# Kernel tuning notes

Hardware: AMD Instinct MI355X
Metric: run time of the kernel (lower is better)

The kernel has to match this reference:

```python
import jax, jax.numpy as jnp
import numpy as np

B, N, D = 32, 128, 64
E = N * N
EPS = 1e-5


def _bn(x, gamma, beta):
    # torch BatchNorm1d on (B, C, D): normalize per-channel over (batch, last dim)
    mean = jnp.mean(x, axis=(0, 2), keepdims=True)
    var = jnp.var(x, axis=(0, 2), keepdims=True)
    return (x - mean) * jax.lax.rsqrt(var + EPS) * gamma[None, :, None] + beta[None, :, None]


def _gat_layer(x, edge, Wh, We, Wp, Wa, gv, bv, ge, be):
    b, n, d = x.shape
    res = x
    z_h = jnp.einsum('bnd,od->bno', x, Wh)   # fc_h (torch Linear: y = x W^T)
    z_e = jnp.einsum('bed,od->beo', edge, We)  # fc_e
    # incidence matmuls are pure gathers: edge e = i*n + j
    z_src = jnp.broadcast_to(z_h[:, None, :, :], (b, n, n, d)).reshape(b, n * n, d)  # start: edge (i,j) <- node j
    z_dst = jnp.broadcast_to(z_h[:, :, None, :], (b, n, n, d)).reshape(b, n * n, d)  # end:   edge (i,j) <- node i
    z = jnp.concatenate([z_src, z_dst, z_e], axis=-1)  # (b, E, 3d)
    z_e_new = jnp.einsum('bec,oc->beo', z, Wp)  # fc_proj
    attn = jnp.einsum('bec,c->be', z, Wa[0])    # attn_fc -> (b, E)
    attn = jnp.where(attn >= 0, attn, 0.01 * attn)  # LeakyReLU(0.01)
    attn = jax.nn.softmax(attn.reshape(b, n, n), axis=2).reshape(b, n * n)  # softmax over sources j
    # scatter via end^T: node i <- sum_j attn[i,j] * z_src[i*n+j]
    agg = (attn[:, :, None] * z_src).reshape(b, n, n, d).sum(axis=2)
    x_new = jax.nn.elu(res + _bn(agg, gv, bv))
    edge_new = jax.nn.elu(_bn(z_e_new, ge, be))
    return x_new, edge_new


def setup_inputs():
    key = jax.random.key(0)
    ks = jax.random.split(key, 10)
    scale = float(np.sqrt(2.0 / D))
    return {
        'x': jax.random.normal(ks[0], (B, N, D), jnp.float32),
        'edge': jax.random.normal(ks[1], (B, E, D), jnp.float32),
        'Wh1': jax.random.normal(ks[2], (D, D), jnp.float32) * scale,
        'We1': jax.random.normal(ks[3], (D, D), jnp.float32) * scale,
        'Wp1': jax.random.normal(ks[4], (D, 3 * D), jnp.float32) * scale,
        'Wa1': jax.random.normal(ks[5], (1, 3 * D), jnp.float32) * scale,
        'Wh2': jax.random.normal(ks[6], (D, D), jnp.float32) * scale,
        'We2': jax.random.normal(ks[7], (D, D), jnp.float32) * scale,
        'Wp2': jax.random.normal(ks[8], (D, 3 * D), jnp.float32) * scale,
        'Wa2': jax.random.normal(ks[9], (1, 3 * D), jnp.float32) * scale,
        'gv1': jnp.ones((N,), jnp.float32), 'bv1': jnp.zeros((N,), jnp.float32),
        'ge1': jnp.ones((E,), jnp.float32), 'be1': jnp.zeros((E,), jnp.float32),
        'gv2': jnp.ones((N,), jnp.float32), 'bv2': jnp.zeros((N,), jnp.float32),
        'ge2': jnp.ones((E,), jnp.float32), 'be2': jnp.zeros((E,), jnp.float32),
    }


def reference(x, edge, Wh1, We1, Wp1, Wa1, Wh2, We2, Wp2, Wa2,
              gv1, bv1, ge1, be1, gv2, bv2, ge2, be2):
    x, edge = _gat_layer(x, edge, Wh1, We1, Wp1, Wa1, gv1, bv1, ge1, be1)
    x, edge = _gat_layer(x, edge, Wh2, We2, Wp2, Wa2, gv2, bv2, ge2, be2)
    return x, edge
```

## Files before the change

### kernel.cpp

```cpp
#include <hip/hip_runtime.h>
#include <math.h>

#define BB 32
#define NN 128
#define DD 64
#define EE (NN*NN)
#define EPSI 1e-5f

typedef __attribute__((ext_vector_type(8))) short bf16x8;
typedef __attribute__((ext_vector_type(4))) short s16x4;
typedef __attribute__((ext_vector_type(4))) float f32x4;

#define LGKM0() do { asm volatile("s_waitcnt lgkmcnt(0)" ::: "memory"); \
                     __builtin_amdgcn_sched_barrier(0); } while (0)

__device__ __forceinline__ short f2bf(float f) {
    union { float f; unsigned u; } v; v.f = f;
    unsigned u = v.u;
    unsigned r = (u + 0x7FFFu + ((u >> 16) & 1u)) >> 16;
    return (short)r;
}
__device__ __forceinline__ float elu(float v) {
    return v > 0.f ? v : __expf(v) - 1.f;
}

__global__ void k_node(const float* __restrict__ x, const float* __restrict__ Wh,
                       const float* __restrict__ Wp, const float* __restrict__ We,
                       const float* __restrict__ Wa,
                       float* __restrict__ zh, float* __restrict__ PsT,
                       float* __restrict__ PdT, float* __restrict__ sO,
                       float* __restrict__ tO,
                       short* __restrict__ MbT, short* __restrict__ wfT)
{
    const int row = blockIdx.x;
    const int d = threadIdx.x;
    if (row >= BB*NN) {
        const int ff = row - BB*NN;
        float acc = 0.f;
        for (int o = 0; o < DD; ++o)
            acc += Wp[ff*192 + 128 + o] * We[o*DD + d];
        MbT[(((ff >> 4)*2 + (d >> 5))*64 + (ff & 15) + ((d >> 3) & 3)*16)*8 + (d & 7)]
            = f2bf(acc);
        if (ff == 0) {
            for (int q = 0; q < 16; ++q) wfT[d*16 + q] = 0;
            __syncthreads();
            float aw = 0.f;
            for (int o = 0; o < DD; ++o)
                aw += Wa[128 + o] * We[o*DD + d];
            wfT[((d >> 5)*64 + ((d >> 3) & 3)*16)*8 + (d & 7)] = f2bf(aw);
        }
        return;
    }
    const int b = row >> 7, n = row & 127;
    __shared__ float xr[DD];
    __shared__ float zr[DD];
    xr[d] = x[row*DD + d];
    __syncthreads();
    float acc = 0.f;
#pragma unroll
    for (int k = 0; k < DD; ++k) acc += xr[k] * Wh[d*DD + k];
    zr[d] = acc;
    zh[row*DD + d] = acc;
    __syncthreads();
    float a0 = 0.f, a1 = 0.f;
#pragma unroll
    for (int o = 0; o < DD; ++o) {
        float z = zr[o];
        a0 += Wp[d*192 + o]      * z;
        a1 += Wp[d*192 + 64 + o] * z;
    }
    const int fi = ((b >> 4)*4 + (d >> 4))*256 + (((b >> 2) & 3)*16 + (d & 15))*4 + (b & 3);
    PsT[n*2048 + fi] = a0;
    PdT[n*2048 + fi] = a1;
    float sv = zr[d] * Wa[d];
    float tv = zr[d] * Wa[64 + d];
#pragma unroll
    for (int off = 32; off; off >>= 1) {
        sv += __shfl_xor(sv, off);
        tv += __shfl_xor(tv, off);
    }
    if (d == 0) { sO[row] = sv; tO[row] = tv; }
}

template <int INM, int OUTM>
__global__ __launch_bounds__(256, 4) void k_edge(
    const void* einv,
    const short* __restrict__ MbT,
    const short* __restrict__ wfT,
    const float* __restrict__ PsT,
    const float* __restrict__ PdT,
    const float* __restrict__ ge, const float* __restrict__ be,
    void* eoutv, float* __restrict__ uout)
{
    __shared__ short As[4][32][72];
    const int t  = threadIdx.x;
    const int l  = t & 63;
    const int wv = t >> 6;
    const int lr = l & 15;
    const int lg = l >> 4;
    const int e0 = blockIdx.x * 4;
    const int e  = e0 + wv;
    const int i0 = e >> 7, j0 = e & 127;

    bf16x8 afr[2][2];
    if constexpr (INM == 0) {
        const float* ein = (const float*)einv;
        const int tq = (t >> 4) & 3;
        const int d0 = (t & 15) * 4;
        float4 sv[8];
#pragma unroll
        for (int it = 0; it < 8; ++it) {
            const int b = it*4 + wv;
            sv[it] = *reinterpret_cast<const float4*>(
                         ein + ((size_t)b*EE + e0 + tq)*DD + d0);
        }
#pragma unroll
        for (int it = 0; it < 8; ++it) {
            const int b = it*4 + wv;
            s16x4 o;
            o[0] = f2bf(sv[it].x); o[1] = f2bf(sv[it].y);
            o[2] = f2bf(sv[it].z); o[3] = f2bf(sv[it].w);
            *reinterpret_cast<s16x4*>(&As[tq][b][d0]) = o;
        }
        __syncthreads();
#pragma unroll
        for (int m = 0; m < 2; ++m)
#pragma unroll
            for (int s = 0; s < 2; ++s)
                afr[m][s] = *reinterpret_cast<const bf16x8*>(
                                &As[wv][16*m + lr][s*32 + lg*8]);
    } else {
        const short* ein = (const short*)einv + (size_t)e*BB*DD;
#pragma unroll
        for (int m = 0; m < 2; ++m)
#pragma unroll
            for (int s = 0; s < 2; ++s)
                afr[m][s] = *reinterpret_cast<const bf16x8*>(
                                ein + ((m*2 + s)*64 + l)*8);
    }

    bf16x8 bfr[4][2];
#pragma unroll
    for (int n = 0; n < 4; ++n)
#pragma unroll
        for (int s = 0; s < 2; ++s)
            bfr[n][s] = *reinterpret_cast<const bf16x8*>(MbT + ((n*2 + s)*64 + l)*8);
    bf16x8 wfrag[2];
#pragma unroll
    for (int s = 0; s < 2; ++s)
        wfrag[s] = *reinterpret_cast<const bf16x8*>(wfT + (s*64 + l)*8);

    f32x4 acc[2][4];
    f32x4 uacc[2];
    {
        const float* psb = PsT + j0*2048;
        const float* pdb = PdT + i0*2048;
#pragma unroll
        for (int m = 0; m < 2; ++m) {
            uacc[m] = (f32x4){0.f, 0.f, 0.f, 0.f};
#pragma unroll
            for (int n = 0; n < 4; ++n) {
                const float4 a = *reinterpret_cast<const float4*>(psb + (m*4+n)*256 + l*4);
                const float4 c = *reinterpret_cast<const float4*>(pdb + (m*4+n)*256 + l*4);
                acc[m][n] = (f32x4){a.x+c.x, a.y+c.y, a.z+c.z, a.w+c.w};
            }
        }
    }

#pragma unroll
    for (int m = 0; m < 2; ++m) {
#pragma unroll
        for (int n = 0; n < 4; ++n)
            acc[m][n] = __builtin_amdgcn_mfma_f32_16x16x32_bf16(afr[m][0], bfr[n][0], acc[m][n], 0, 0, 0);
        uacc[m] = __builtin_amdgcn_mfma_f32_16x16x32_bf16(afr[m][0], wfrag[0], uacc[m], 0, 0, 0);
#pragma unroll
        for (int n = 0; n < 4; ++n)
            acc[m][n] = __builtin_amdgcn_mfma_f32_16x16x32_bf16(afr[m][1], bfr[n][1], acc[m][n], 0, 0, 0);
        uacc[m] = __builtin_amdgcn_mfma_f32_16x16x32_bf16(afr[m][1], wfrag[1], uacc[m], 0, 0, 0);
    }

    float s1 = 0.f, s2 = 0.f;
#pragma unroll
    for (int m = 0; m < 2; ++m)
#pragma unroll
        for (int n = 0; n < 4; ++n)
#pragma unroll
            for (int q = 0; q < 4; ++q) { float v = acc[m][n][q]; s1 += v; s2 += v*v; }
#pragma unroll
    for (int off = 1; off < 64; off <<= 1) {
        s1 += __shfl_xor(s1, off);
        s2 += __shfl_xor(s2, off);
    }
    const float mean = s1 * (1.f/2048.f);
    const float var  = s2 * (1.f/2048.f) - mean*mean;
    const float sc = ge[e] * rsqrtf(var + EPSI);
    const float sh = be[e] - mean*sc;

#pragma unroll
    for (int m = 0; m < 2; ++m)
#pragma unroll
        for (int n = 0; n < 4; ++n)
#pragma unroll
            for (int q = 0; q < 4; ++q)
                acc[m][n][q] = elu(acc[m][n][q]*sc + sh);

    if (lr == 0) {
#pragma unroll
        for (int m = 0; m < 2; ++m)
#pragma unroll
            for (int q = 0; q < 4; ++q)
                uout[(size_t)(16*m + 4*lg + q)*EE + e] = uacc[m][q];
    }

    float (*Z)[68] = reinterpret_cast<float (*)[68]>(&As[wv][0][0]);
    LGKM0();
#pragma unroll
    for (int h = 0; h < 2; ++h) {
#pragma unroll
        for (int n = 0; n < 4; ++n)
#pragma unroll
            for (int q = 0; q < 4; ++q)
                Z[4*lg + q][16*n + lr] = acc[h][n][q];
        LGKM0();
        if constexpr (OUTM == 0) {
            float* eout = (float*)eoutv;
#pragma unroll
            for (int it = 0; it < 4; ++it) {
                const int rr = lg + 4*it;
                const int b  = 16*h + rr;
                float4 z = *reinterpret_cast<float4*>(&Z[rr][lr*4]);
                *reinterpret_cast<float4*>(eout + ((size_t)b*EE + e)*DD + lr*4) = z;
            }
        } else {
            short* eoutp = (short*)eoutv + (size_t)e*BB*DD;
#pragma unroll
            for (int it = 0; it < 2; ++it) {
                const int rr = (l >> 3) + 8*it;
                const int c0 = (l & 7)*8;
                float4 zlo = *reinterpret_cast<float4*>(&Z[rr][c0]);
                float4 zhi = *reinterpret_cast<float4*>(&Z[rr][c0+4]);
                bf16x8 o;
                o[0]=f2bf(zlo.x); o[1]=f2bf(zlo.y); o[2]=f2bf(zlo.z); o[3]=f2bf(zlo.w);
                o[4]=f2bf(zhi.x); o[5]=f2bf(zhi.y); o[6]=f2bf(zhi.z); o[7]=f2bf(zhi.w);
                const int sp = (l & 7) >> 2;
                const int lp = rr + ((l & 3) << 4);
                *reinterpret_cast<bf16x8*>(eoutp + ((h*2 + sp)*64 + lp)*8) = o;
            }
        }
        LGKM0();
    }
}

__global__ void k_attn(const float* __restrict__ sI, const float* __restrict__ tI,
                       const float* __restrict__ u, const float* __restrict__ zh,
                       float* __restrict__ agg)
{
    int blk = blockIdx.x; int b = blk >> 7, i = blk & 127;
    int l = threadIdx.x;
    __shared__ float at[NN];
    float ti = tI[blk];
    float l0 = sI[b*NN + l]      + ti + u[b*EE + i*NN + l];
    float l1 = sI[b*NN + l + 64] + ti + u[b*EE + i*NN + l + 64];
    l0 = l0 >= 0.f ? l0 : 0.01f*l0;
    l1 = l1 >= 0.f ? l1 : 0.01f*l1;
    float mx = fmaxf(l0, l1);
#pragma unroll
    for (int off = 32; off; off >>= 1) mx = fmaxf(mx, __shfl_xor(mx, off));
    float e0 = __expf(l0 - mx), e1 = __expf(l1 - mx);
    float sm = e0 + e1;
#pragma unroll
    for (int off = 32; off; off >>= 1) sm += __shfl_xor(sm, off);
    float inv = 1.f / sm;
    at[l]      = e0 * inv;
    at[l + 64] = e1 * inv;
    __syncthreads();
    const float* zb = zh + (size_t)b*NN*DD + l;
    float a0 = 0.f, a1 = 0.f, a2 = 0.f, a3 = 0.f;
#pragma unroll 4
    for (int j = 0; j < NN; j += 4) {
        a0 += at[j]     * zb[(j)    *DD];
        a1 += at[j + 1] * zb[(j + 1)*DD];
        a2 += at[j + 2] * zb[(j + 2)*DD];
        a3 += at[j + 3] * zb[(j + 3)*DD];
    }
    agg[(b*NN + i)*DD + l] = (a0 + a1) + (a2 + a3);
}

__global__ void k_vbn(const float* __restrict__ agg, const float* __restrict__ xres,
                      const float* __restrict__ gv, const float* __restrict__ bv,
                      float* __restrict__ xout)
{
    int i = blockIdx.x, t = threadIdx.x;
    float vals[8];
    float s1 = 0.f, s2 = 0.f;
#pragma unroll
    for (int q = 0; q < 8; ++q) {
        int m = t + 256*q; int b = m >> 6, d = m & 63;
        float v = agg[(b*NN + i)*DD + d];
        vals[q] = v; s1 += v; s2 += v*v;
    }
#pragma unroll
    for (int off = 1; off < 64; off <<= 1) {
        s1 += __shfl_xor(s1, off);
        s2 += __shfl_xor(s2, off);
    }
    __shared__ float r1[4], r2[4];
    int wv = t >> 6;
    if ((t & 63) == 0) { r1[wv] = s1; r2[wv] = s2; }
    __syncthreads();
    s1 = r1[0] + r1[1] + r1[2] + r1[3];
    s2 = r2[0] + r2[1] + r2[2] + r2[3];
    float mean  = s1 * (1.f/2048.f);
    float var   = s2 * (1.f/2048.f) - mean*mean;
    float scale = gv[i] * rsqrtf(var + EPSI);
    float shift = bv[i] - mean*scale;
#pragma unroll
    for (int q = 0; q < 8; ++q) {
        int m = t + 256*q; int b = m >> 6, d = m & 63;
        float v = vals[q]*scale + shift + xres[(b*NN + i)*DD + d];
        xout[(b*NN + i)*DD + d] = v > 0.f ? v : __expf(v) - 1.f;
    }
}

extern "C" void kernel_launch(void* const* d_in, const int* in_sizes, int n_in,
                              void* d_out, int out_size, void* d_ws, size_t ws_size,
                              hipStream_t stream)
{
    const float* x    = (const float*)d_in[0];
    const float* edge = (const float*)d_in[1];
    const float* Wh1  = (const float*)d_in[2];
    const float* We1  = (const float*)d_in[3];
    const float* Wp1  = (const float*)d_in[4];
    const float* Wa1  = (const float*)d_in[5];
    const float* Wh2  = (const float*)d_in[6];
    const float* We2  = (const float*)d_in[7];
    const float* Wp2  = (const float*)d_in[8];
    const float* Wa2  = (const float*)d_in[9];
    const float* gv1  = (const float*)d_in[10];
    const float* bv1  = (const float*)d_in[11];
    const float* ge1  = (const float*)d_in[12];
    const float* be1  = (const float*)d_in[13];
    const float* gv2  = (const float*)d_in[14];
    const float* bv2  = (const float*)d_in[15];
    const float* ge2  = (const float*)d_in[16];
    const float* be2  = (const float*)d_in[17];

    float* xout = (float*)d_out;
    float* eout = (float*)d_out + BB*NN*DD;

    float* ws  = (float*)d_ws;
    short* MbT = (short*)ws;  ws += DD*DD/2;
    short* wfT = (short*)ws;  ws += 1024/2;
    float* zh  = ws;  ws += BB*NN*DD;
    float* PsT = ws;  ws += NN*BB*DD;
    float* PdT = ws;  ws += NN*BB*DD;
    float* sb  = ws;  ws += BB*NN;
    float* tb  = ws;  ws += BB*NN;
    float* ub  = ws;  ws += BB*EE;
    float* agg = ws;  ws += BB*NN*DD;
    float* x1  = ws;  ws += BB*NN*DD;
    short* ebf = (short*)ws;
    const size_t need = ((size_t)(ws - (float*)d_ws))*4 + (size_t)EE*BB*DD*2;

    const bool dense = (ws_size >= need);

    k_node<<<BB*NN + 64, 64, 0, stream>>>(x, Wh1, Wp1, We1, Wa1, zh, PsT, PdT, sb, tb, MbT, wfT);
    if (dense)
        k_edge<0,1><<<EE/4, 256, 0, stream>>>(edge, MbT, wfT, PsT, PdT, ge1, be1, ebf, ub);
    else
        k_edge<0,0><<<EE/4, 256, 0, stream>>>(edge, MbT, wfT, PsT, PdT, ge1, be1, eout, ub);
    k_attn<<<BB*NN, 64, 0, stream>>>(sb, tb, ub, zh, agg);
    k_vbn<<<NN, 256, 0, stream>>>(agg, x, gv1, bv1, x1);
    k_node<<<BB*NN + 64, 64, 0, stream>>>(x1, Wh2, Wp2, We2, Wa2, zh, PsT, PdT, sb, tb, MbT, wfT);
    if (dense)
        k_edge<1,0><<<EE/4, 256, 0, stream>>>(ebf, MbT, wfT, PsT, PdT, ge2, be2, eout, ub);
    else
        k_edge<0,0><<<EE/4, 256, 0, stream>>>(eout, MbT, wfT, PsT, PdT, ge2, be2, eout, ub);
    k_attn<<<BB*NN, 64, 0, stream>>>(sb, tb, ub, zh, agg);
    k_vbn<<<NN, 256, 0, stream>>>(agg, x1, gv2, bv2, xout);
}
```

Before: 182.7 us.

## Make k_edge waves independent, use DPP reductions and single-pass output staging

Each wave now loads its own edge's 32x64 input tile instead of the block cooperatively loading four edges. This removes the block-wide __syncthreads, and the per-wave shared region is enlarged so all 32 rows of the fp32 output fit at once, which makes the epilogue one pass. The 64-lane shuffle-xor reductions for the batch-norm statistics are replaced with DPP row shifts/broadcasts plus readlane. The trade-off is a different global load pattern: each wave reads 16 lanes per contiguous 256-byte row instead of the previous coalescing across 4 adjacent edges, plus a larger LDS footprint per block.

Result: slower. 187.6 us (+2.7%).

```diff
diff --git a/kernel.cpp b/kernel.cpp
--- a/kernel.cpp
+++ b/kernel.cpp
@@ -13,6 +13,20 @@
 
 #define LGKM0() do { asm volatile("s_waitcnt lgkmcnt(0)" ::: "memory"); \
                      __builtin_amdgcn_sched_barrier(0); } while (0)
+
+#define DPPADD(v, ctrl, rmask)                                               \
+    (v) += __int_as_float(__builtin_amdgcn_update_dpp(                       \
+               0, __float_as_int(v), (ctrl), (rmask), 0xf, true))
+
+__device__ __forceinline__ float wave_sum64(float v) {
+    DPPADD(v, 0x111, 0xf);
+    DPPADD(v, 0x112, 0xf);
+    DPPADD(v, 0x114, 0xf);
+    DPPADD(v, 0x118, 0xf);
+    DPPADD(v, 0x142, 0xa);
+    DPPADD(v, 0x143, 0xc);
+    return __int_as_float(__builtin_amdgcn_readlane(__float_as_int(v), 63));
+}
 
 __device__ __forceinline__ short f2bf(float f) {
     union { float f; unsigned u; } v; v.f = f;
@@ -92,43 +106,42 @@
     const float* __restrict__ ge, const float* __restrict__ be,
     void* eoutv, float* __restrict__ uout)
 {
-    __shared__ short As[4][32][72];
+    __shared__ __align__(16) char SM[4][8704];
     const int t  = threadIdx.x;
     const int l  = t & 63;
     const int wv = t >> 6;
     const int lr = l & 15;
     const int lg = l >> 4;
-    const int e0 = blockIdx.x * 4;
-    const int e  = e0 + wv;
+    const int e  = blockIdx.x * 4 + wv;
     const int i0 = e >> 7, j0 = e & 127;
+    short (*As)[72] = reinterpret_cast<short (*)[72]>(&SM[wv][0]);
+    float (*Z)[68]  = reinterpret_cast<float (*)[68]>(&SM[wv][0]);
 
     bf16x8 afr[2][2];
     if constexpr (INM == 0) {
         const float* ein = (const float*)einv;
-        const int tq = (t >> 4) & 3;
-        const int d0 = (t & 15) * 4;
         float4 sv[8];
 #pragma unroll
         for (int it = 0; it < 8; ++it) {
-            const int b = it*4 + wv;
+            const int b = 4*it + (l >> 4);
             sv[it] = *reinterpret_cast<const float4*>(
-                         ein + ((size_t)b*EE + e0 + tq)*DD + d0);
+                         ein + ((size_t)b*EE + e)*DD + (l & 15)*4);
         }
 #pragma unroll
         for (int it = 0; it < 8; ++it) {
-            const int b = it*4 + wv;
+            const int b = 4*it + (l >> 4);
             s16x4 o;
             o[0] = f2bf(sv[it].x); o[1] = f2bf(sv[it].y);
             o[2] = f2bf(sv[it].z); o[3] = f2bf(sv[it].w);
-            *reinterpret_cast<s16x4*>(&As[tq][b][d0]) = o;
-        }
-        __syncthreads();
+            *reinterpret_cast<s16x4*>(&As[b][(l & 15)*4]) = o;
+        }
+        LGKM0();
 #pragma unroll
         for (int m = 0; m < 2; ++m)
 #pragma unroll
             for (int s = 0; s < 2; ++s)
                 afr[m][s] = *reinterpret_cast<const bf16x8*>(
-                                &As[wv][16*m + lr][s*32 + lg*8]);
+                                &As[16*m + lr][s*32 + lg*8]);
     } else {
         const short* ein = (const short*)einv + (size_t)e*BB*DD;
 #pragma unroll
@@ -186,11 +199,8 @@
         for (int n = 0; n < 4; ++n)
 #pragma unroll
             for (int q = 0; q < 4; ++q) { float v = acc[m][n][q]; s1 += v; s2 += v*v; }
-#pragma unroll
-    for (int off = 1; off < 64; off <<= 1) {
-        s1 += __shfl_xor(s1, off);
-        s2 += __shfl_xor(s2, off);
-    }
+    s1 = wave_sum64(s1);
+    s2 = wave_sum64(s2);
     const float mean = s1 * (1.f/2048.f);
     const float var  = s2 * (1.f/2048.f) - mean*mean;
     const float sc = ge[e] * rsqrtf(var + EPSI);
@@ -212,42 +222,38 @@
                 uout[(size_t)(16*m + 4*lg + q)*EE + e] = uacc[m][q];
     }
 
-    float (*Z)[68] = reinterpret_cast<float (*)[68]>(&As[wv][0][0]);
     LGKM0();
 #pragma unroll
-    for (int h = 0; h < 2; ++h) {
+    for (int m = 0; m < 2; ++m)
 #pragma unroll
         for (int n = 0; n < 4; ++n)
 #pragma unroll
             for (int q = 0; q < 4; ++q)
-                Z[4*lg + q][16*n + lr] = acc[h][n][q];
-        LGKM0();
-        if constexpr (OUTM == 0) {
-            float* eout = (float*)eoutv;
-#pragma unroll
-            for (int it = 0; it < 4; ++it) {
-                const int rr = lg + 4*it;
-                const int b  = 16*h + rr;
-                float4 z = *reinterpret_cast<float4*>(&Z[rr][lr*4]);
-                *reinterpret_cast<float4*>(eout + ((size_t)b*EE + e)*DD + lr*4) = z;
-            }
-        } else {
-            short* eoutp = (short*)eoutv + (size_t)e*BB*DD;
-#pragma unroll
-            for (int it = 0; it < 2; ++it) {
-                const int rr = (l >> 3) + 8*it;
-                const int c0 = (l & 7)*8;
-                float4 zlo = *reinterpret_cast<float4*>(&Z[rr][c0]);
-                float4 zhi = *reinterpret_cast<float4*>(&Z[rr][c0+4]);
-                bf16x8 o;
-                o[0]=f2bf(zlo.x); o[1]=f2bf(zlo.y); o[2]=f2bf(zlo.z); o[3]=f2bf(zlo.w);
-                o[4]=f2bf(zhi.x); o[5]=f2bf(zhi.y); o[6]=f2bf(zhi.z); o[7]=f2bf(zhi.w);
-                const int sp = (l & 7) >> 2;
-                const int lp = rr + ((l & 3) << 4);
-                *reinterpret_cast<bf16x8*>(eoutp + ((h*2 + sp)*64 + lp)*8) = o;
-            }
-        }
-        LGKM0();
+                Z[16*m + 4*lg + q][16*n + lr] = acc[m][n][q];
+    LGKM0();
+    if constexpr (OUTM == 0) {
+        float* eout = (float*)eoutv;
+#pragma unroll
+        for (int it = 0; it < 8; ++it) {
+            const int b = lg + 4*it;
+            float4 z = *reinterpret_cast<float4*>(&Z[b][lr*4]);
+            *reinterpret_cast<float4*>(eout + ((size_t)b*EE + e)*DD + lr*4) = z;
+        }
+    } else {
+        short* eoutp = (short*)eoutv + (size_t)e*BB*DD;
+#pragma unroll
+        for (int it = 0; it < 4; ++it) {
+            const int b  = (l >> 3) + 8*it;
+            const int c0 = (l & 7)*8;
+            float4 zlo = *reinterpret_cast<float4*>(&Z[b][c0]);
+            float4 zhi = *reinterpret_cast<float4*>(&Z[b][c0+4]);
+            bf16x8 o;
+            o[0]=f2bf(zlo.x); o[1]=f2bf(zlo.y); o[2]=f2bf(zlo.z); o[3]=f2bf(zlo.w);
+            o[4]=f2bf(zhi.x); o[5]=f2bf(zhi.y); o[6]=f2bf(zhi.z); o[7]=f2bf(zhi.w);
+            const int sp = (l & 7) >> 2;
+            const int lp = (b & 15) + ((l & 3) << 4);
+            *reinterpret_cast<bf16x8*>(eoutp + (((b >> 4)*2 + sp)*64 + lp)*8) = o;
+        }
     }
 }
 
```
